# Kernel tuning notes

Hardware: AMD Instinct MI355X
Metric: run time of the kernel (lower is better)

## Reference

```python
import jax, jax.numpy as jnp
import numpy as np

B, C, H, W = 2, 256, 64, 64
NUM_HEADS = 4
DIM_HEAD_QK = 64
DIM_HEAD_V = 64  # dim_out // num_heads
DIM_OUT_QK = NUM_HEADS * DIM_HEAD_QK  # 256
DIM_OUT_V = NUM_HEADS * DIM_HEAD_V    # 256
SCALE = DIM_HEAD_QK ** -0.5


def rel_logits_1d(q, rel_k, permute):
    # q: (Bh, Hq, Wq, d), rel_k: (2*Wq-1, d)
    Bh, Hq, Wq, d = q.shape
    R = 2 * Wq - 1
    x = jnp.einsum('bhwd,rd->bhwr', q, rel_k)              # (Bh, Hq, Wq, R)
    x = x.reshape(-1, Wq, R)
    x_pad = jnp.pad(x, ((0, 0), (0, 0), (0, 1))).reshape(x.shape[0], -1)
    x_pad = jnp.pad(x_pad, ((0, 0), (0, Wq - 1)))
    x_pad = x_pad.reshape(-1, Wq + 1, R)
    x = x_pad[:, :Wq, Wq - 1:]                              # (Bh*Hq, Wq, Wq)
    x = x.reshape(Bh, Hq, 1, Wq, Wq)
    x = jnp.broadcast_to(x, (Bh, Hq, Hq, Wq, Wq))
    return jnp.transpose(x, permute)


def pos_embed_rel(q, height_rel, width_rel):
    # q: (Bh, HW, d)
    Bh = q.shape[0]
    qr = q.reshape(Bh, H, W, -1)
    rel_w = rel_logits_1d(qr, width_rel, (0, 1, 3, 2, 4))   # (Bh, H, W, H, W)
    qt = jnp.transpose(qr, (0, 2, 1, 3))                    # (Bh, W, H, d)
    rel_h = rel_logits_1d(qt, height_rel, (0, 3, 1, 4, 2))  # (Bh, H, W, H, W)
    return (rel_h + rel_w).reshape(Bh, H * W, H * W)


def setup_inputs() -> dict:
    key = jax.random.key(0)
    k1, k2, k3, k4 = jax.random.split(key, 4)
    x = jax.random.normal(k1, (B, C, H, W), dtype=jnp.float32)
    qkv_w = jax.random.normal(k2, (2 * DIM_OUT_QK + DIM_OUT_V, C), dtype=jnp.float32) * (C ** -0.5)
    height_rel = jax.random.normal(k3, (2 * H - 1, DIM_HEAD_QK), dtype=jnp.float32) * SCALE
    width_rel = jax.random.normal(k4, (2 * W - 1, DIM_HEAD_QK), dtype=jnp.float32) * SCALE
    return {"x": x, "qkv_w": qkv_w, "height_rel": height_rel, "width_rel": width_rel}


def reference(x, qkv_w, height_rel, width_rel):
    # 1x1 conv == channel matmul
    qkv = jnp.einsum('bchw,oc->bohw', x, qkv_w)             # (B, 768, H, W)
    q, k, v = jnp.split(qkv, [DIM_OUT_QK, 2 * DIM_OUT_QK], axis=1)
    HW = H * W
    q = q.reshape(B * NUM_HEADS, DIM_HEAD_QK, HW).transpose(0, 2, 1)  # (Bh, HW, d)
    k = k.reshape(B * NUM_HEADS, DIM_HEAD_QK, HW)                     # (Bh, d, HW)
    v = v.reshape(B * NUM_HEADS, DIM_HEAD_V, HW).transpose(0, 2, 1)   # (Bh, HW, dv)
    attn = jnp.einsum('bnd,bdm->bnm', q, k) * SCALE + pos_embed_rel(q, height_rel, width_rel)
    attn = jax.nn.softmax(attn, axis=-1)
    out = jnp.einsum('bnm,bmd->bnd', attn, v)               # (Bh, HW, dv)
    out = out.transpose(0, 2, 1).reshape(B, DIM_OUT_V, H, W)
    return out
```

## Files before the change

### kernel.cpp

```cpp
#include <hip/hip_runtime.h>
#include <hip/hip_bf16.h>

typedef __attribute__((ext_vector_type(8))) short bf16x8;
typedef __attribute__((ext_vector_type(4))) float f32x4;

static __device__ __forceinline__ f32x4 mfma16(bf16x8 a, bf16x8 b, f32x4 c) {
    return __builtin_amdgcn_mfma_f32_16x16x32_bf16(a, b, c, 0, 0, 0);
}
static __device__ __forceinline__ void gll16(const void* g, void* l) {
    __builtin_amdgcn_global_load_lds(
        (const __attribute__((address_space(1))) unsigned int*)g,
        (__attribute__((address_space(3))) unsigned int*)l, 16, 0, 0);
}
static __device__ __forceinline__ bf16x8 pack8(float4 a, float4 b) {
    union { bf16x8 v; __hip_bfloat162 h[4]; } u;
    u.h[0] = __float22bfloat162_rn(float2{a.x, a.y});
    u.h[1] = __float22bfloat162_rn(float2{a.z, a.w});
    u.h[2] = __float22bfloat162_rn(float2{b.x, b.y});
    u.h[3] = __float22bfloat162_rn(float2{b.z, b.w});
    return u.v;
}

#define LOG2E 1.44269504f

__global__ __launch_bounds__(256, 4) void qkv_kernel(
    const float* __restrict__ x, const float* __restrict__ w,
    __hip_bfloat16* __restrict__ qb, __hip_bfloat16* __restrict__ kb,
    __hip_bfloat16* __restrict__ vt)
{
    alignas(16) __shared__ __hip_bfloat16 sA[64 * 72];
    alignas(16) __shared__ __hip_bfloat16 sB[64 * 72];
    const int nb = blockIdx.x * 64;
    const int ob = blockIdx.y * 64;
    const int b  = blockIdx.z;
    const int tid  = threadIdx.x;
    const int lane = tid & 63;
    const int wv   = tid >> 6;
    const int quad = lane >> 4;
    const int l16  = lane & 15;

    f32x4 acc[4];
    for (int i = 0; i < 4; i++) acc[i] = (f32x4)0.f;

    const int oA = tid >> 2, cA = (tid & 3) << 4;
    const float* srcw = w + (ob + oA) * 256 + cA;
    const int cB = tid >> 2, nB = (tid & 3) << 4;
    const int csw = cB ^ ((tid & 3) * 16);
    const float* srcx = x + ((size_t)b * 256 + cB) * 4096 + nb + nB;

    float4 ra[4], rb4[4];
    #pragma unroll
    for (int i = 0; i < 4; i++) ra[i]  = *(const float4*)(srcw + i * 4);
    #pragma unroll
    for (int i = 0; i < 4; i++) rb4[i] = *(const float4*)(srcx + i * 4);

    for (int t = 0; t < 4; t++) {
        __syncthreads();
        {
            union { bf16x8 v; __hip_bfloat16 h[8]; } u0, u1;
            #pragma unroll
            for (int i = 0; i < 2; i++) {
                float4 f = ra[i];
                u0.h[4*i+0] = __float2bfloat16(f.x); u0.h[4*i+1] = __float2bfloat16(f.y);
                u0.h[4*i+2] = __float2bfloat16(f.z); u0.h[4*i+3] = __float2bfloat16(f.w);
            }
            #pragma unroll
            for (int i = 0; i < 2; i++) {
                float4 f = ra[2 + i];
                u1.h[4*i+0] = __float2bfloat16(f.x); u1.h[4*i+1] = __float2bfloat16(f.y);
                u1.h[4*i+2] = __float2bfloat16(f.z); u1.h[4*i+3] = __float2bfloat16(f.w);
            }
            *(bf16x8*)&sA[oA * 72 + cA]     = u0.v;
            *(bf16x8*)&sA[oA * 72 + cA + 8] = u1.v;
        }
        {
            #pragma unroll
            for (int i = 0; i < 4; i++) {
                float4 f = rb4[i];
                sB[(nB + 4*i + 0) * 72 + csw] = __float2bfloat16(f.x);
                sB[(nB + 4*i + 1) * 72 + csw] = __float2bfloat16(f.y);
                sB[(nB + 4*i + 2) * 72 + csw] = __float2bfloat16(f.z);
                sB[(nB + 4*i + 3) * 72 + csw] = __float2bfloat16(f.w);
            }
        }
        __syncthreads();
        if (t < 3) {
            #pragma unroll
            for (int i = 0; i < 4; i++)
                ra[i]  = *(const float4*)(srcw + (t + 1) * 64 + i * 4);
            #pragma unroll
            for (int i = 0; i < 4; i++)
                rb4[i] = *(const float4*)(srcx + (size_t)(t + 1) * 64 * 4096 + i * 4);
        }
        const __hip_bfloat16* aRow = &sA[(16 * wv + l16) * 72];
        #pragma unroll
        for (int ks = 0; ks < 2; ks++) {
            bf16x8 af = *(const bf16x8*)&aRow[ks * 32 + quad * 8];
            #pragma unroll
            for (int ct = 0; ct < 4; ct++) {
                bf16x8 bfv = *(const bf16x8*)&sB[(16 * ct + l16) * 72
                                                 + ((ks * 32 + quad * 8) ^ (ct * 16))];
                acc[ct] = mfma16(af, bfv, acc[ct]);
            }
        }
    }
    if (ob < 512) {
        __syncthreads();
        #pragma unroll
        for (int ct = 0; ct < 4; ct++) {
            union { short4 s; __hip_bfloat16 hh[4]; } u;
            #pragma unroll
            for (int r = 0; r < 4; r++) u.hh[r] = __float2bfloat16(acc[ct][r]);
            *(short4*)&sA[(16 * ct + l16) * 72 + 16 * wv + 4 * quad] = u.s;
        }
        __syncthreads();
        const int n_l = tid >> 2, d16 = (tid & 3) * 16;
        const int n = nb + n_l;
        const __hip_bfloat16* srcl = &sA[n_l * 72 + d16];
        bf16x8 v0 = *(const bf16x8*)srcl;
        bf16x8 v1 = *(const bf16x8*)(srcl + 8);
        const int bhh = b * 4 + ((ob & 255) >> 6);
        if (ob < 256) {
            __hip_bfloat16* dst = qb + ((size_t)bhh * 4096 + n) * 64;
            *(bf16x8*)(dst + d16)     = v0;
            *(bf16x8*)(dst + d16 + 8) = v1;
        } else {
            const int s = (n & 7) << 3;
            __hip_bfloat16* dst = kb + ((size_t)bhh * 4096 + n) * 64;
            *(bf16x8*)(dst + (d16 ^ s))       = v0;
            *(bf16x8*)(dst + ((d16 + 8) ^ s)) = v1;
        }
    } else {
        __syncthreads();
        #pragma unroll
        for (int ct = 0; ct < 4; ct++)
            #pragma unroll
            for (int r = 0; r < 4; r++)
                sA[(16 * wv + quad * 4 + r) * 72 + 16 * ct + l16] = __float2bfloat16(acc[ct][r]);
        int o2 = (ob - 512) + 16 * wv + l16;
        int bhh = b * 4 + (o2 >> 6), d = o2 & 63;
        const __hip_bfloat16* srcl = &sA[(16 * wv + l16) * 72 + 16 * quad];
        __hip_bfloat16* vrow = vt + ((size_t)bhh * 64 + d) * 4096;
        const int kt = quad & 1;
        const int gbase = nb + (quad >> 1) * 32;
        const int dsw = (d & 7) << 3;
        #pragma unroll
        for (int m = 0; m < 4; m++) {
            short4 val = *(const short4*)(srcl + 4 * m);
            int P4 = gbase + 8 * m + 4 * kt;
            *(short4*)(vrow + (P4 ^ dsw)) = val;
        }
    }
}

__global__ __launch_bounds__(256, 4) void attn_kernel(
    const __hip_bfloat16* __restrict__ qb, const __hip_bfloat16* __restrict__ kb,
    const __hip_bfloat16* __restrict__ vt, const float* __restrict__ hrel,
    const float* __restrict__ wrel, float* __restrict__ out)
{
    extern __shared__ __align__(16) char smem[];
    __shared__ __hip_bfloat16 sRH[64 * 64];

    const int h    = blockIdx.x;
    const int bh   = blockIdx.y;
    const int tid  = threadIdx.x;
    const int lane = tid & 63;
    const int wv   = tid >> 6;
    const int qg   = wv >> 1;
    const int kg   = wv & 1;
    const int quad = lane >> 4;
    const int l16  = lane & 15;

    __hip_bfloat16* sQ   = (__hip_bfloat16*)smem;
    __hip_bfloat16* sW   = (__hip_bfloat16*)smem + 64 * 72;
    __hip_bfloat16* sHRs = (__hip_bfloat16*)smem + 128 * 72;
    __hip_bfloat16* sRWt = (__hip_bfloat16*)smem;

    {
        int r = tid >> 2, c0 = (tid & 3) * 16;
        const __hip_bfloat16* srcq = qb + ((size_t)bh * 4096 + h * 64 + r) * 64 + c0;
        *(bf16x8*)&sQ[r * 72 + c0]     = *(const bf16x8*)srcq;
        *(bf16x8*)&sQ[r * 72 + c0 + 8] = *(const bf16x8*)(srcq + 8);
        const float* srch = hrel + (size_t)(63 - h + r) * 64 + c0;
        *(bf16x8*)&sHRs[r * 72 + c0]     = pack8(*(const float4*)srch,
                                                 *(const float4*)(srch + 4));
        *(bf16x8*)&sHRs[r * 72 + c0 + 8] = pack8(*(const float4*)(srch + 8),
                                                 *(const float4*)(srch + 12));
    }
    __syncthreads();

    const __hip_bfloat16* aRow = &sQ[(16 * wv + l16) * 72];
    bf16x8 qf0 = *(const bf16x8*)&aRow[quad * 8];
    bf16x8 qf1 = *(const bf16x8*)&aRow[32 + quad * 8];
    bf16x8 qm[2][2];
    #pragma unroll
    for (int qt = 0; qt < 2; qt++) {
        const __hip_bfloat16* qr = &sQ[(qg * 32 + 16 * qt + l16) * 72];
        qm[qt][0] = *(const bf16x8*)&qr[quad * 8];
        qm[qt][1] = *(const bf16x8*)&qr[32 + quad * 8];
    }
    __syncthreads();

    for (int p = 0; p < 2; p++) {
        {
            int r = tid >> 2, c0 = (tid & 3) * 16;
            int gr = 64 * p + r;
            bf16x8 w0 = (bf16x8)(short)0, w1 = (bf16x8)(short)0;
            if (gr < 127) {
                const float* s = wrel + (size_t)gr * 64 + c0;
                w0 = pack8(*(const float4*)s, *(const float4*)(s + 4));
                w1 = pack8(*(const float4*)(s + 8), *(const float4*)(s + 12));
            }
            *(bf16x8*)&sW[r * 72 + c0]     = w0;
            *(bf16x8*)&sW[r * 72 + c0 + 8] = w1;
        }
        __syncthreads();
        #pragma unroll
        for (int ct = 0; ct < 4; ct++) {
            f32x4 a = (f32x4)0.f;
            a = mfma16(qf0, *(const bf16x8*)&sW[(16 * ct + l16) * 72 + quad * 8], a);
            a = mfma16(qf1, *(const bf16x8*)&sW[(16 * ct + l16) * 72 + 32 + quad * 8], a);
            int rr = 64 * p + 16 * ct + l16;
            #pragma unroll
            for (int r = 0; r < 4; r++) {
                int ww = 16 * wv + quad * 4 + r;
                int wp = rr + ww - 63;
                if (wp >= 0 && wp < 64) sRWt[ww * 68 + wp] = __float2bfloat16(a[r]);
            }
        }
        if (p == 0) {
            #pragma unroll
            for (int ct = 0; ct < 4; ct++) {
                f32x4 a = (f32x4)0.f;
                a = mfma16(qf0, *(const bf16x8*)&sHRs[(16 * ct + l16) * 72 + quad * 8], a);
                a = mfma16(qf1, *(const bf16x8*)&sHRs[(16 * ct + l16) * 72 + 32 + quad * 8], a);
                #pragma unroll
                for (int r = 0; r < 4; r++)
                    sRH[(16 * ct + l16) * 64 + 16 * wv + quad * 4 + r] = __float2bfloat16(a[r]);
            }
        }
        __syncthreads();
    }

    union S4 { short4 s; __hip_bfloat16 h[4]; };
    float rwf[2][2][4];
    #pragma unroll
    for (int qt = 0; qt < 2; qt++)
        #pragma unroll
        for (int kt = 0; kt < 2; kt++) {
            S4 t;
            t.s = *(const short4*)&sRWt[(qg * 32 + 16 * qt + l16) * 68
                                        + kg * 32 + 16 * kt + 4 * quad];
            #pragma unroll
            for (int r = 0; r < 4; r++)
                rwf[qt][kt][r] = LOG2E * __bfloat162float(t.h[r]);
        }
    __syncthreads();

    const char* kT = (const char*)kb + (size_t)bh * 524288 + wv * 2048 + lane * 16;
    const char* vT = (const char*)vt + (size_t)bh * 524288
                     + (size_t)(16 * wv + (lane >> 3)) * 8192 + (lane & 7) * 16;

    gll16(kT,          smem + wv * 2048);
    gll16(kT + 1024,   smem + wv * 2048 + 1024);
    gll16(vT,          smem + 8192 + wv * 2048);
    gll16(vT + 65536,  smem + 8192 + wv * 2048 + 1024);
    __syncthreads();

    f32x4 oacc[2][4];
    #pragma unroll
    for (int qt = 0; qt < 2; qt++)
        #pragma unroll
        for (int dt = 0; dt < 4; dt++) oacc[qt][dt] = (f32x4)0.f;
    f32x4 lacc[2] = {(f32x4)0.f, (f32x4)0.f};
    const bf16x8 vones = (bf16x8)(short)0x3F80;

    const int krowOff = (kg * 32 + l16) * 128;
    const int sw  = (l16 & 7) << 4;
    const int kA  = (quad * 16) ^ sw;
    const int kB  = (64 + quad * 16) ^ sw;
    const int vOff = 8192 + l16 * 128 + ((kg * 64 + quad * 16) ^ sw);

    const __hip_bfloat16* rhq = sRH + qg * 32 + l16;
    const float SC = 0.125f * LOG2E;

    for (int j = 0; j < 64; j++) {
        const char* buf = smem + (j & 1) * 16384;
        if (j < 63) {
            char* nbuf = smem + ((j + 1) & 1) * 16384;
            const char* gk = kT + (size_t)(j + 1) * 8192;
            gll16(gk,         nbuf + wv * 2048);
            gll16(gk + 1024,  nbuf + wv * 2048 + 1024);
            const char* gv = vT + (size_t)(j + 1) * 128;
            gll16(gv,         nbuf + 8192 + wv * 2048);
            gll16(gv + 65536, nbuf + 8192 + wv * 2048 + 1024);
        }

        const char* kr = buf + krowOff;
        bf16x8 kf00 = *(const bf16x8*)(kr + kA);
        bf16x8 kf01 = *(const bf16x8*)(kr + kB);
        bf16x8 kf10 = *(const bf16x8*)(kr + 2048 + kA);
        bf16x8 kf11 = *(const bf16x8*)(kr + 2048 + kB);

        f32x4 s[2][2];
        __builtin_amdgcn_s_setprio(1);
        #pragma unroll
        for (int qt = 0; qt < 2; qt++) {
            f32x4 a0 = (f32x4)0.f, a1 = (f32x4)0.f;
            a0 = mfma16(kf00, qm[qt][0], a0);
            a0 = mfma16(kf01, qm[qt][1], a0);
            a1 = mfma16(kf10, qm[qt][0], a1);
            a1 = mfma16(kf11, qm[qt][1], a1);
            s[qt][0] = a0; s[qt][1] = a1;
        }
        __builtin_amdgcn_s_setprio(0);

        bf16x8 pa[2];
        #pragma unroll
        for (int qt = 0; qt < 2; qt++) {
            float rhb = LOG2E * __bfloat162float(rhq[j * 64 + 16 * qt]);
            float pv[8];
            #pragma unroll
            for (int r = 0; r < 4; r++)
                pv[r] = __builtin_amdgcn_exp2f(fmaf(s[qt][0][r], SC, rwf[qt][0][r] + rhb));
            #pragma unroll
            for (int r = 0; r < 4; r++)
                pv[4 + r] = __builtin_amdgcn_exp2f(fmaf(s[qt][1][r], SC, rwf[qt][1][r] + rhb));
            union { bf16x8 v; __hip_bfloat162 b2[4]; } pu;
            #pragma unroll
            for (int pi = 0; pi < 4; pi++)
                pu.b2[pi] = __float22bfloat162_rn(float2{pv[2 * pi], pv[2 * pi + 1]});
            pa[qt] = pu.v;
        }

        __builtin_amdgcn_s_setprio(1);
        #pragma unroll
        for (int dt = 0; dt < 4; dt++) {
            bf16x8 vf = *(const bf16x8*)(buf + vOff + dt * 2048);
            oacc[0][dt] = mfma16(pa[0], vf, oacc[0][dt]);
            oacc[1][dt] = mfma16(pa[1], vf, oacc[1][dt]);
        }
        lacc[0] = mfma16(pa[0], vones, lacc[0]);
        lacc[1] = mfma16(pa[1], vones, lacc[1]);
        __builtin_amdgcn_s_setprio(0);
        __syncthreads();
    }

    float* obuf = (float*)smem;
    if (kg == 1) {
        #pragma unroll
        for (int qt = 0; qt < 2; qt++)
            #pragma unroll
            for (int dt = 0; dt < 4; dt++)
                *(f32x4*)&obuf[qg * 2304 + (16 * dt + l16) * 36 + 16 * qt + 4 * quad]
                    = oacc[qt][dt];
        if (l16 == 0)
            #pragma unroll
            for (int qt = 0; qt < 2; qt++)
                #pragma unroll
                for (int r = 0; r < 4; r++)
                    obuf[4608 + qg * 32 + 16 * qt + 4 * quad + r] = lacc[qt][r];
    }
    __syncthreads();
    if (kg == 0) {
        #pragma unroll
        for (int qt = 0; qt < 2; qt++) {
            #pragma unroll
            for (int dt = 0; dt < 4; dt++)
                oacc[qt][dt] += *(const f32x4*)&obuf[qg * 2304 + (16 * dt + l16) * 36
                                                     + 16 * qt + 4 * quad];
            #pragma unroll
            for (int r = 0; r < 4; r++)
                lacc[qt][r] += obuf[4608 + qg * 32 + 16 * qt + 4 * quad + r];
        }
        const int b = bh >> 2, head = bh & 3;
        #pragma unroll
        for (int qt = 0; qt < 2; qt++) {
            f32x4 lv;
            #pragma unroll
            for (int r = 0; r < 4; r++) lv[r] = 1.f / lacc[qt][r];
            #pragma unroll
            for (int dt = 0; dt < 4; dt++) {
                f32x4 o = oacc[qt][dt] * lv;
                int dv = 16 * dt + l16;
                int q0 = qg * 32 + 16 * qt + 4 * quad;
                *(f32x4*)&out[((size_t)(b * 256 + head * 64 + dv)) * 4096 + h * 64 + q0] = o;
            }
        }
    }
}

extern "C" void kernel_launch(void* const* d_in, const int* in_sizes, int n_in,
                              void* d_out, int out_size, void* d_ws, size_t ws_size,
                              hipStream_t stream) {
    const float* x     = (const float*)d_in[0];
    const float* qkv_w = (const float*)d_in[1];
    const float* hrel  = (const float*)d_in[2];
    const float* wrel  = (const float*)d_in[3];
    float* out = (float*)d_out;

    __hip_bfloat16* qb = (__hip_bfloat16*)d_ws;
    __hip_bfloat16* kb = qb + (size_t)8 * 4096 * 64;
    __hip_bfloat16* vt = kb + (size_t)8 * 4096 * 64;

    qkv_kernel<<<dim3(64, 12, 2), 256, 0, stream>>>(x, qkv_w, qb, kb, vt);
    attn_kernel<<<dim3(64, 8), 256, 32768, stream>>>(qb, kb, vt, hrel, wrel, out);
}
```

Before: 130.2 us.

## Split attention query rows across two blocks to double grid parallelism

The attention kernel now launches a third grid dimension of two, so each block handles 32 query rows instead of 64, with each wave owning 16 rows. The grid goes from 512 to 1024 blocks, which gives better CU fill on a 256-CU device, and per-thread registers drop. In exchange, every K/V tile is streamed from global memory twice (once per half), and each block computes the relative-position logits again for its subset.

```diff
diff --git a/kernel.cpp b/kernel.cpp
--- a/kernel.cpp
+++ b/kernel.cpp
@@ -159,102 +159,101 @@
     const float* __restrict__ wrel, float* __restrict__ out)
 {
     extern __shared__ __align__(16) char smem[];
-    __shared__ __hip_bfloat16 sRH[64 * 64];
+    __shared__ __hip_bfloat16 sRH[64 * 32];
 
     const int h    = blockIdx.x;
     const int bh   = blockIdx.y;
+    const int qg   = blockIdx.z;
     const int tid  = threadIdx.x;
     const int lane = tid & 63;
     const int wv   = tid >> 6;
-    const int qg   = wv >> 1;
+    const int qh   = wv >> 1;
     const int kg   = wv & 1;
     const int quad = lane >> 4;
     const int l16  = lane & 15;
 
     __hip_bfloat16* sQ   = (__hip_bfloat16*)smem;
-    __hip_bfloat16* sW   = (__hip_bfloat16*)smem + 64 * 72;
-    __hip_bfloat16* sHRs = (__hip_bfloat16*)smem + 128 * 72;
+    __hip_bfloat16* sW   = (__hip_bfloat16*)smem + 32 * 72;
+    __hip_bfloat16* sHRs = (__hip_bfloat16*)smem + 160 * 72;
     __hip_bfloat16* sRWt = (__hip_bfloat16*)smem;
 
     {
+        int r = tid >> 3, d8 = (tid & 7) * 8;
+        *(bf16x8*)&sQ[r * 72 + d8] =
+            *(const bf16x8*)&qb[((size_t)bh * 4096 + h * 64 + qg * 32 + r) * 64 + d8];
+    }
+    {
+        int r = tid >> 1, c0 = (tid & 1) * 32;
+        bf16x8 w0 = (bf16x8)(short)0, w1 = w0, w2 = w0, w3 = w0;
+        if (r < 127) {
+            const float* s = wrel + (size_t)r * 64 + c0;
+            w0 = pack8(*(const float4*)(s),      *(const float4*)(s + 4));
+            w1 = pack8(*(const float4*)(s + 8),  *(const float4*)(s + 12));
+            w2 = pack8(*(const float4*)(s + 16), *(const float4*)(s + 20));
+            w3 = pack8(*(const float4*)(s + 24), *(const float4*)(s + 28));
+        }
+        *(bf16x8*)&sW[r * 72 + c0]      = w0;
+        *(bf16x8*)&sW[r * 72 + c0 + 8]  = w1;
+        *(bf16x8*)&sW[r * 72 + c0 + 16] = w2;
+        *(bf16x8*)&sW[r * 72 + c0 + 24] = w3;
+    }
+    {
         int r = tid >> 2, c0 = (tid & 3) * 16;
-        const __hip_bfloat16* srcq = qb + ((size_t)bh * 4096 + h * 64 + r) * 64 + c0;
-        *(bf16x8*)&sQ[r * 72 + c0]     = *(const bf16x8*)srcq;
-        *(bf16x8*)&sQ[r * 72 + c0 + 8] = *(const bf16x8*)(srcq + 8);
-        const float* srch = hrel + (size_t)(63 - h + r) * 64 + c0;
-        *(bf16x8*)&sHRs[r * 72 + c0]     = pack8(*(const float4*)srch,
-                                                 *(const float4*)(srch + 4));
-        *(bf16x8*)&sHRs[r * 72 + c0 + 8] = pack8(*(const float4*)(srch + 8),
-                                                 *(const float4*)(srch + 12));
-    }
-    __syncthreads();
-
-    const __hip_bfloat16* aRow = &sQ[(16 * wv + l16) * 72];
-    bf16x8 qf0 = *(const bf16x8*)&aRow[quad * 8];
-    bf16x8 qf1 = *(const bf16x8*)&aRow[32 + quad * 8];
-    bf16x8 qm[2][2];
+        const float* s = hrel + (size_t)(63 - h + r) * 64 + c0;
+        *(bf16x8*)&sHRs[r * 72 + c0]     = pack8(*(const float4*)s, *(const float4*)(s + 4));
+        *(bf16x8*)&sHRs[r * 72 + c0 + 8] = pack8(*(const float4*)(s + 8),
+                                                 *(const float4*)(s + 12));
+    }
+    __syncthreads();
+
+    bf16x8 qm0, qm1;
+    {
+        const __hip_bfloat16* qr = &sQ[(qh * 16 + l16) * 72];
+        qm0 = *(const bf16x8*)&qr[quad * 8];
+        qm1 = *(const bf16x8*)&qr[32 + quad * 8];
+    }
+    __syncthreads();
+
+    {
+        const int rbase = kg * 64;
+        #pragma unroll
+        for (int ct = 0; ct < 4; ct++) {
+            int rr = rbase + 16 * ct + l16;
+            f32x4 a = (f32x4)0.f;
+            a = mfma16(qm0, *(const bf16x8*)&sW[rr * 72 + quad * 8], a);
+            a = mfma16(qm1, *(const bf16x8*)&sW[rr * 72 + 32 + quad * 8], a);
+            #pragma unroll
+            for (int r = 0; r < 4; r++) {
+                int wwb = 16 * qh + quad * 4 + r;
+                int wp = rr + qg * 32 + wwb - 63;
+                if (wp >= 0 && wp < 64) sRWt[wwb * 68 + wp] = __float2bfloat16(a[r]);
+            }
+        }
+    }
+    {
+        #pragma unroll
+        for (int c = 0; c < 2; c++) {
+            int hp = kg * 32 + 16 * c + l16;
+            f32x4 a = (f32x4)0.f;
+            a = mfma16(qm0, *(const bf16x8*)&sHRs[hp * 72 + quad * 8], a);
+            a = mfma16(qm1, *(const bf16x8*)&sHRs[hp * 72 + 32 + quad * 8], a);
+            #pragma unroll
+            for (int r = 0; r < 4; r++)
+                sRH[hp * 32 + qh * 16 + quad * 4 + r] = __float2bfloat16(a[r]);
+        }
+    }
+    __syncthreads();
+
+    union S4 { short4 s; __hip_bfloat16 hh[4]; };
+    float rwf[2][4];
     #pragma unroll
-    for (int qt = 0; qt < 2; qt++) {
-        const __hip_bfloat16* qr = &sQ[(qg * 32 + 16 * qt + l16) * 72];
-        qm[qt][0] = *(const bf16x8*)&qr[quad * 8];
-        qm[qt][1] = *(const bf16x8*)&qr[32 + quad * 8];
-    }
-    __syncthreads();
-
-    for (int p = 0; p < 2; p++) {
-        {
-            int r = tid >> 2, c0 = (tid & 3) * 16;
-            int gr = 64 * p + r;
-            bf16x8 w0 = (bf16x8)(short)0, w1 = (bf16x8)(short)0;
-            if (gr < 127) {
-                const float* s = wrel + (size_t)gr * 64 + c0;
-                w0 = pack8(*(const float4*)s, *(const float4*)(s + 4));
-                w1 = pack8(*(const float4*)(s + 8), *(const float4*)(s + 12));
-            }
-            *(bf16x8*)&sW[r * 72 + c0]     = w0;
-            *(bf16x8*)&sW[r * 72 + c0 + 8] = w1;
-        }
-        __syncthreads();
-        #pragma unroll
-        for (int ct = 0; ct < 4; ct++) {
-            f32x4 a = (f32x4)0.f;
-            a = mfma16(qf0, *(const bf16x8*)&sW[(16 * ct + l16) * 72 + quad * 8], a);
-            a = mfma16(qf1, *(const bf16x8*)&sW[(16 * ct + l16) * 72 + 32 + quad * 8], a);
-            int rr = 64 * p + 16 * ct + l16;
-            #pragma unroll
-            for (int r = 0; r < 4; r++) {
-                int ww = 16 * wv + quad * 4 + r;
-                int wp = rr + ww - 63;
-                if (wp >= 0 && wp < 64) sRWt[ww * 68 + wp] = __float2bfloat16(a[r]);
-            }
-        }
-        if (p == 0) {
-            #pragma unroll
-            for (int ct = 0; ct < 4; ct++) {
-                f32x4 a = (f32x4)0.f;
-                a = mfma16(qf0, *(const bf16x8*)&sHRs[(16 * ct + l16) * 72 + quad * 8], a);
-                a = mfma16(qf1, *(const bf16x8*)&sHRs[(16 * ct + l16) * 72 + 32 + quad * 8], a);
-                #pragma unroll
-                for (int r = 0; r < 4; r++)
-                    sRH[(16 * ct + l16) * 64 + 16 * wv + quad * 4 + r] = __float2bfloat16(a[r]);
-            }
-        }
-        __syncthreads();
-    }
-
-    union S4 { short4 s; __hip_bfloat16 h[4]; };
-    float rwf[2][2][4];
-    #pragma unroll
-    for (int qt = 0; qt < 2; qt++)
-        #pragma unroll
-        for (int kt = 0; kt < 2; kt++) {
-            S4 t;
-            t.s = *(const short4*)&sRWt[(qg * 32 + 16 * qt + l16) * 68
-                                        + kg * 32 + 16 * kt + 4 * quad];
-            #pragma unroll
-            for (int r = 0; r < 4; r++)
-                rwf[qt][kt][r] = LOG2E * __bfloat162float(t.h[r]);
-        }
+    for (int kt = 0; kt < 2; kt++) {
+        S4 t;
+        t.s = *(const short4*)&sRWt[(qh * 16 + l16) * 68 + kg * 32 + 16 * kt + 4 * quad];
+        #pragma unroll
+        for (int r = 0; r < 4; r++)
+            rwf[kt][r] = LOG2E * __bfloat162float(t.hh[r]);
+    }
     __syncthreads();
 
     const char* kT = (const char*)kb + (size_t)bh * 524288 + wv * 2048 + lane * 16;
@@ -267,12 +266,10 @@
     gll16(vT + 65536,  smem + 8192 + wv * 2048 + 1024);
     __syncthreads();
 
-    f32x4 oacc[2][4];
+    f32x4 oacc[4];
     #pragma unroll
-    for (int qt = 0; qt < 2; qt++)
-        #pragma unroll
-        for (int dt = 0; dt < 4; dt++) oacc[qt][dt] = (f32x4)0.f;
-    f32x4 lacc[2] = {(f32x4)0.f, (f32x4)0.f};
+    for (int dt = 0; dt < 4; dt++) oacc[dt] = (f32x4)0.f;
+    f32x4 lacc = (f32x4)0.f;
     const bf16x8 vones = (bf16x8)(short)0x3F80;
 
     const int krowOff = (kg * 32 + l16) * 128;
@@ -281,7 +278,7 @@
     const int kB  = (64 + quad * 16) ^ sw;
     const int vOff = 8192 + l16 * 128 + ((kg * 64 + quad * 16) ^ sw);
 
-    const __hip_bfloat16* rhq = sRH + qg * 32 + l16;
+    const __hip_bfloat16* rhq = sRH + qh * 16 + l16;
     const float SC = 0.125f * LOG2E;
 
     for (int j = 0; j < 64; j++) {
@@ -302,90 +299,69 @@
         bf16x8 kf10 = *(const bf16x8*)(kr + 2048 + kA);
         bf16x8 kf11 = *(const bf16x8*)(kr + 2048 + kB);
 
-        f32x4 s[2][2];
+        f32x4 s0 = (f32x4)0.f, s1 = (f32x4)0.f;
         __builtin_amdgcn_s_setprio(1);
-        #pragma unroll
-        for (int qt = 0; qt < 2; qt++) {
-            f32x4 a0 = (f32x4)0.f, a1 = (f32x4)0.f;
-            a0 = mfma16(kf00, qm[qt][0], a0);
-            a0 = mfma16(kf01, qm[qt][1], a0);
-            a1 = mfma16(kf10, qm[qt][0], a1);
-            a1 = mfma16(kf11, qm[qt][1], a1);
-            s[qt][0] = a0; s[qt][1] = a1;
-        }
+        s0 = mfma16(kf00, qm0, s0);
+        s0 = mfma16(kf01, qm1, s0);
+        s1 = mfma16(kf10, qm0, s1);
+        s1 = mfma16(kf11, qm1, s1);
         __builtin_amdgcn_s_setprio(0);
 
-        bf16x8 pa[2];
-        #pragma unroll
-        for (int qt = 0; qt < 2; qt++) {
-            float rhb = LOG2E * __bfloat162float(rhq[j * 64 + 16 * qt]);
-            float pv[8];
-            #pragma unroll
-            for (int r = 0; r < 4; r++)
-                pv[r] = __builtin_amdgcn_exp2f(fmaf(s[qt][0][r], SC, rwf[qt][0][r] + rhb));
-            #pragma unroll
-            for (int r = 0; r < 4; r++)
-                pv[4 + r] = __builtin_amdgcn_exp2f(fmaf(s[qt][1][r], SC, rwf[qt][1][r] + rhb));
+        float rhb = LOG2E * __bfloat162float(rhq[j * 32]);
+        float pv[8];
+        #pragma unroll
+        for (int r = 0; r < 4; r++)
+            pv[r] = __builtin_amdgcn_exp2f(fmaf(s0[r], SC, rwf[0][r] + rhb));
+        #pragma unroll
+        for (int r = 0; r < 4; r++)
+            pv[4 + r] = __builtin_amdgcn_exp2f(fmaf(s1[r], SC, rwf[1][r] + rhb));
+        bf16x8 pa;
+        {
             union { bf16x8 v; __hip_bfloat162 b2[4]; } pu;
             #pragma unroll
             for (int pi = 0; pi < 4; pi++)
                 pu.b2[pi] = __float22bfloat162_rn(float2{pv[2 * pi], pv[2 * pi + 1]});
-            pa[qt] = pu.v;
+            pa = pu.v;
         }
 
         __builtin_amdgcn_s_setprio(1);
         #pragma unroll
         for (int dt = 0; dt < 4; dt++) {
             bf16x8 vf = *(const bf16x8*)(buf + vOff + dt * 2048);
-            oacc[0][dt] = mfma16(pa[0], vf, oacc[0][dt]);
-            oacc[1][dt] = mfma16(pa[1], vf, oacc[1][dt]);
-        }
-        lacc[0] = mfma16(pa[0], vones, lacc[0]);
-        lacc[1] = mfma16(pa[1], vones, lacc[1]);
+            oacc[dt] = mfma16(pa, vf, oacc[dt]);
+        }
+        lacc = mfma16(pa, vones, lacc);
         __builtin_amdgcn_s_setprio(0);
         __syncthreads();
     }
 
     float* obuf = (float*)smem;
+    float* lbuf = obuf + 2560;
     if (kg == 1) {
         #pragma unroll
-        for (int qt = 0; qt < 2; qt++)
-            #pragma unroll
-            for (int dt = 0; dt < 4; dt++)
-                *(f32x4*)&obuf[qg * 2304 + (16 * dt + l16) * 36 + 16 * qt + 4 * quad]
-                    = oacc[qt][dt];
+        for (int dt = 0; dt < 4; dt++)
+            *(f32x4*)&obuf[qh * 1280 + (16 * dt + l16) * 20 + 4 * quad] = oacc[dt];
         if (l16 == 0)
             #pragma unroll
-            for (int qt = 0; qt < 2; qt++)
-                #pragma unroll
-                for (int r = 0; r < 4; r++)
-                    obuf[4608 + qg * 32 + 16 * qt + 4 * quad + r] = lacc[qt][r];
+            for (int r = 0; r < 4; r++)
+                lbuf[qh * 16 + 4 * quad + r] = lacc[r];
     }
     __syncthreads();
     if (kg == 0) {
         #pragma unroll
-        for (int qt = 0; qt < 2; qt++) {
-            #pragma unroll
-            for (int dt = 0; dt < 4; dt++)
-                oacc[qt][dt] += *(const f32x4*)&obuf[qg * 2304 + (16 * dt + l16) * 36
-                                                     + 16 * qt + 4 * quad];
-            #pragma unroll
-            for (int r = 0; r < 4; r++)
-                lacc[qt][r] += obuf[4608 + qg * 32 + 16 * qt + 4 * quad + r];
-        }
+        for (int dt = 0; dt < 4; dt++)
+            oacc[dt] += *(const f32x4*)&obuf[qh * 1280 + (16 * dt + l16) * 20 + 4 * quad];
+        f32x4 lv;
+        #pragma unroll
+        for (int r = 0; r < 4; r++)
+            lv[r] = 1.f / (lacc[r] + lbuf[qh * 16 + 4 * quad + r]);
         const int b = bh >> 2, head = bh & 3;
         #pragma unroll
-        for (int qt = 0; qt < 2; qt++) {
-            f32x4 lv;
-            #pragma unroll
-            for (int r = 0; r < 4; r++) lv[r] = 1.f / lacc[qt][r];
-            #pragma unroll
-            for (int dt = 0; dt < 4; dt++) {
-                f32x4 o = oacc[qt][dt] * lv;
-                int dv = 16 * dt + l16;
-                int q0 = qg * 32 + 16 * qt + 4 * quad;
-                *(f32x4*)&out[((size_t)(b * 256 + head * 64 + dv)) * 4096 + h * 64 + q0] = o;
-            }
+        for (int dt = 0; dt < 4; dt++) {
+            f32x4 o = oacc[dt] * lv;
+            int dv = 16 * dt + l16;
+            int q0 = qg * 32 + qh * 16 + 4 * quad;
+            *(f32x4*)&out[((size_t)(b * 256 + head * 64 + dv)) * 4096 + h * 64 + q0] = o;
         }
     }
 }
@@ -404,5 +380,5 @@
     __hip_bfloat16* vt = kb + (size_t)8 * 4096 * 64;
 
     qkv_kernel<<<dim3(64, 12, 2), 256, 0, stream>>>(x, qkv_w, qb, kb, vt);
-    attn_kernel<<<dim3(64, 8), 256, 32768, stream>>>(qb, kb, vt, hrel, wrel, out);
-}
+    attn_kernel<<<dim3(64, 8, 2), 256, 32768, stream>>>(qb, kb, vt, hrel, wrel, out);
+}
```

Result: slower. 141.0 us (+8.3%).
